# Kernel tuning notes

Hardware: AMD Instinct MI355X
Metric: run time of the kernel (lower is better)

## Reference

```python
import jax, jax.numpy as jnp
import numpy as np

N = 50000          # nodes
E = 1600000        # edges (avg degree 32)
F_IN = 128         # input feature dim
H = 8              # attention heads
D = 8              # per-head dim (concat -> H*D = 64)
NEG_SLOPE = 0.2    # PyG GATConv leaky relu slope


def setup_inputs() -> dict:
    key = jax.random.key(0)
    ks = jax.random.split(key, 16)
    x = jax.random.normal(ks[0], (N, F_IN), jnp.float32)
    edge_index = jax.random.randint(ks[1], (2, E), 0, N, jnp.int32)
    inp = {"x": x, "edge_index": edge_index}
    fin = F_IN
    for i in range(4):
        inp[f"W{i}"] = jax.random.normal(ks[2 + 3 * i], (fin, H * D), jnp.float32) * (1.0 / np.sqrt(fin))
        inp[f"att{i}"] = jax.random.normal(ks[3 + 3 * i], (2, H, D), jnp.float32) * 0.1
        inp[f"b{i}"] = jnp.zeros((H * D,), jnp.float32)
        fin = H * D
    return inp


def gat_layer(x, W, att, b, src, dst):
    # linear projection -> per-head features [N, H, D]
    h = (x @ W).reshape(-1, H, D)
    # per-node attention logits for src/dst roles [N, H]
    e_src = jnp.einsum("nhd,hd->nh", h, att[0])
    e_dst = jnp.einsum("nhd,hd->nh", h, att[1])
    # per-edge score [E, H]
    e = jax.nn.leaky_relu(e_src[src] + e_dst[dst], NEG_SLOPE)
    # segment softmax over incoming edges of each dst node
    m = jax.ops.segment_max(e, dst, num_segments=N)
    w = jnp.exp(e - m[dst])
    s = jax.ops.segment_sum(w, dst, num_segments=N)
    alpha = w / (s[dst] + 1e-16)
    # weighted message scatter-add: [E,H,D] -> [N,H,D]
    msg = alpha[:, :, None] * h[src]
    out = jax.ops.segment_sum(msg, dst, num_segments=N)
    return out.reshape(-1, H * D) + b


def reference(x, edge_index, W0, att0, b0, W1, att1, b1, W2, att2, b2, W3, att3, b3):
    src, dst = edge_index[0], edge_index[1]
    h = x
    params = [(W0, att0, b0), (W1, att1, b1), (W2, att2, b2), (W3, att3, b3)]
    for i, (W, att, b) in enumerate(params):
        h = gat_layer(h, W, att, b, src, dst)
        if i < len(params) - 1:
            h = jax.nn.elu(h)  # inter-layer activation as in PyG GAT (default ELU)
    return h
```

## Files before the change

### kernel.cpp

```cpp
#include <hip/hip_runtime.h>

#define N_NODES 50000
#define N_EDGES 1600000
#define HD 64
#define NH 8
#define NBKT 196
#define EPB 8192
#define GB1 196
#define SCAN_M (NBKT * GB1)
#define NB2 151
#define DCAP 8960
#define SEGB 2048
#define GBN 196

__device__ inline int wave_incl_scan(int v, int lane) {
#pragma unroll
    for (int o = 1; o < 64; o <<= 1) {
        int t = __shfl_up(v, o);
        if (lane >= o) v += t;
    }
    return v;
}

template <int F>
__device__ __forceinline__ void gemm_body16(
    int bx, int by, int t,
    const float* __restrict__ x, const float* __restrict__ W,
    const float* __restrict__ att,
    _Float16* __restrict__ h, float* __restrict__ es, float* __restrict__ ed) {
    int n = bx * 256 + t;
    int f0 = by * 16;
    int nc = (n < N_NODES) ? n : (N_NODES - 1);
    const float4* xrow = (const float4*)x + (size_t)nc * (F / 4);
    float acc[16];
#pragma unroll
    for (int i = 0; i < 16; i++) acc[i] = 0.f;
#pragma unroll 4
    for (int kk = 0; kk < F / 4; kk++) {
        float4 xv = xrow[kk];
        const float* Wk = W + (kk * 4) * 64 + f0;
#pragma unroll
        for (int i = 0; i < 16; i++)
            acc[i] += xv.x * Wk[i] + xv.y * Wk[64 + i] +
                      xv.z * Wk[128 + i] + xv.w * Wk[192 + i];
    }
    if (n >= N_NODES) return;

    float s0 = 0.f, s1 = 0.f, d0 = 0.f, d1 = 0.f;
#pragma unroll
    for (int i = 0; i < 8; i++) {
        s0 += acc[i] * att[f0 + i];
        d0 += acc[i] * att[64 + f0 + i];
    }
#pragma unroll
    for (int i = 8; i < 16; i++) {
        s1 += acc[i] * att[f0 + i];
        d1 += acc[i] * att[64 + f0 + i];
    }
    int hh = f0 >> 3;
    es[n * NH + hh] = s0; es[n * NH + hh + 1] = s1;
    ed[n * NH + hh] = d0; ed[n * NH + hh + 1] = d1;

    union { _Float16 hf[16]; uint4 u[2]; } cv;
#pragma unroll
    for (int i = 0; i < 16; i++) cv.hf[i] = (_Float16)acc[i];
    uint4* hp = (uint4*)(h + (size_t)n * HD + f0);
    hp[0] = cv.u[0];
    hp[1] = cv.u[1];
}

template <int F>
__global__ __launch_bounds__(256) void gemm_att_kernel(
    const float* __restrict__ x, const float* __restrict__ W,
    const float* __restrict__ att,
    _Float16* __restrict__ h, float* __restrict__ es, float* __restrict__ ed) {
    gemm_body16<F>(blockIdx.x, blockIdx.y, threadIdx.x, x, W, att, h, es, ed);
}

__global__ __launch_bounds__(256) void histA_gemm_kernel(
    const int* __restrict__ dst, int* __restrict__ offs,
    const float* __restrict__ x, const float* __restrict__ W,
    const float* __restrict__ att,
    _Float16* __restrict__ h, float* __restrict__ es, float* __restrict__ ed) {
    if (blockIdx.y < 4) {
        gemm_body16<128>(blockIdx.x, blockIdx.y, threadIdx.x, x, W, att, h, es, ed);
        return;
    }
    int bb = blockIdx.x;
    __shared__ int hist[NBKT];
    int t = threadIdx.x;
    if (t < NBKT) hist[t] = 0;
    __syncthreads();
    int base = bb * EPB;
#pragma unroll
    for (int k = 0; k < EPB / 256; k++) {
        int e = base + k * 256 + t;
        if (e < N_EDGES) atomicAdd(&hist[dst[e] >> 8], 1);
    }
    __syncthreads();
    if (t < NBKT) offs[t * GB1 + bb] = hist[t];
}

__global__ __launch_bounds__(256) void scanB1_kernel(int* __restrict__ offs,
                                                     int* __restrict__ part2) {
    __shared__ int wsum[4];
    int t = threadIdx.x, lane = t & 63, wv = t >> 6;
    int i = blockIdx.x * 256 + t;
    int v = (i < SCAN_M) ? offs[i] : 0;
    int inc = wave_incl_scan(v, lane);
    if (lane == 63) wsum[wv] = inc;
    __syncthreads();
    if (t == 0) {
        int a = 0;
        for (int k = 0; k < 4; k++) { int x = wsum[k]; wsum[k] = a; a += x; }
    }
    __syncthreads();
    int excl = wsum[wv] + inc - v;
    if (i < SCAN_M) offs[i] = excl;
    if (t == 255) part2[blockIdx.x] = wsum[wv] + inc;
}

__global__ __launch_bounds__(256) void scatC_kernel(const int* __restrict__ src,
                                                    const int* __restrict__ dst,
                                                    const int* __restrict__ offs,
                                                    const int* __restrict__ part2,
                                                    unsigned* __restrict__ ebuf) {
    __shared__ int cur[NBKT];
    __shared__ int base_s[NBKT];
    __shared__ int p2s[256];
    __shared__ int p2w[4];
    int t = threadIdx.x, lane = t & 63, wv = t >> 6;
    int v = (t < NB2) ? part2[t] : 0;
    int inc = wave_incl_scan(v, lane);
    if (lane == 63) p2w[wv] = inc;
    __syncthreads();
    if (t == 0) {
        int a = 0;
        for (int k = 0; k < 4; k++) { int x = p2w[k]; p2w[k] = a; a += x; }
    }
    __syncthreads();
    p2s[t] = p2w[wv] + inc - v;
    if (t < NBKT) cur[t] = 0;
    __syncthreads();
    if (t < NBKT) {
        int f = t * GB1 + blockIdx.x;
        base_s[t] = offs[f] + p2s[f >> 8];
    }
    __syncthreads();
    int base = blockIdx.x * EPB;
#pragma unroll
    for (int k = 0; k < EPB / 256; k++) {
        int e = base + k * 256 + t;
        if (e < N_EDGES) {
            int d = dst[e];
            int b = d >> 8;
            int r = atomicAdd(&cur[b], 1);
            ebuf[base_s[b] + r] = (unsigned)src[e] | ((unsigned)(d & 255) << 16);
        }
    }
}

__global__ __launch_bounds__(512) void csrD_kernel(const int* __restrict__ offs,
                                                   const int* __restrict__ part2,
                                                   const unsigned* __restrict__ ebuf,
                                                   int* __restrict__ rowptr,
                                                   unsigned short* __restrict__ csr) {
    __shared__ unsigned eb[DCAP];
    __shared__ int hist[SEGB];
    __shared__ int wsum[8];
    __shared__ int p2s[512];
    int b = blockIdx.x, t = threadIdx.x;
    int lane = t & 63, wv = t >> 6;
    {
        int v = (t < NB2) ? part2[t] : 0;
        int inc = wave_incl_scan(v, lane);
        if (lane == 63) wsum[wv] = inc;
        __syncthreads();
        if (t == 0) {
            int a = 0;
            for (int k = 0; k < 8; k++) { int x = wsum[k]; wsum[k] = a; a += x; }
        }
        __syncthreads();
        p2s[t] = wsum[wv] + inc - v;
        __syncthreads();
    }
    int f0 = b * GB1;
    int base = offs[f0] + p2s[f0 >> 8];
    int nxt;
    if (b == NBKT - 1) nxt = N_EDGES;
    else { int f1 = (b + 1) * GB1; nxt = offs[f1] + p2s[f1 >> 8]; }
    int nb = nxt - base;
    if (nb > DCAP) nb = DCAP;
    for (int i = t; i < SEGB; i += 512) hist[i] = 0;
    __syncthreads();
    for (int i = t; i < nb; i += 512) {
        unsigned v = ebuf[base + i];
        eb[i] = v;
        int bin = (int)((v >> 16) << 3) | (int)((v & 0xFFFFu) >> 13);
        atomicAdd(&hist[bin], 1);
    }
    __syncthreads();
    int b0 = t << 2;
    int loc0 = hist[b0], loc1 = hist[b0 + 1], loc2 = hist[b0 + 2], loc3 = hist[b0 + 3];
    int s = loc0 + loc1 + loc2 + loc3;
    int inc = wave_incl_scan(s, lane);
    if (lane == 63) wsum[wv] = inc;
    __syncthreads();
    if (t == 0) {
        int a = 0;
        for (int k = 0; k < 8; k++) { int x = wsum[k]; wsum[k] = a; a += x; }
    }
    __syncthreads();
    int run = wsum[wv] + inc - s;
    hist[b0] = run; run += loc0;
    hist[b0 + 1] = run; run += loc1;
    hist[b0 + 2] = run; run += loc2;
    hist[b0 + 3] = run;
    __syncthreads();
    if (t < 256) {
        int node = b * 256 + t;
        if (node < N_NODES) rowptr[node] = base + hist[t << 3];
    }
    if (b == 0 && t == 0) rowptr[N_NODES] = N_EDGES;
    __syncthreads();
    for (int i = t; i < nb; i += 512) {
        unsigned v = eb[i];
        int bin = (int)((v >> 16) << 3) | (int)((v & 0xFFFFu) >> 13);
        int r = atomicAdd(&hist[bin], 1);
        csr[base + r] = (unsigned short)(v & 0xFFFFu);
    }
}

__global__ __launch_bounds__(256) void agg_kernel(
    const uint4* __restrict__ h8, const float* __restrict__ es,
    const float* __restrict__ ed, const int* __restrict__ rowptr,
    const unsigned short* __restrict__ csr, const float4* __restrict__ b4,
    float4* __restrict__ out4, int apply_elu) {
    int t = threadIdx.x;
    int wv = t >> 6, L = t & 63;
    int n = blockIdx.x * 4 + wv;
    if (n >= N_NODES) return;
    int g = L >> 3, o = L & 7;
    int beg = rowptr[n], end = rowptr[n + 1];
    float edn = ed[n * NH + o];
    float acc[8] = {0.f, 0.f, 0.f, 0.f, 0.f, 0.f, 0.f, 0.f};
    float ssum = 0.f;
    int j = beg;
    for (; j + 32 <= end; j += 32) {
        int s0 = csr[j + g];
        int s1 = csr[j + 8 + g];
        int s2 = csr[j + 16 + g];
        int s3 = csr[j + 24 + g];
        uint4 hv0 = h8[s0 * 8 + o];
        uint4 hv1 = h8[s1 * 8 + o];
        uint4 hv2 = h8[s2 * 8 + o];
        uint4 hv3 = h8[s3 * 8 + o];
        float ev0 = es[s0 * NH + o];
        float ev1 = es[s1 * NH + o];
        float ev2 = es[s2 * NH + o];
        float ev3 = es[s3 * NH + o];
        float e0 = ev0 + edn; e0 = (e0 > 0.f) ? e0 : 0.2f * e0;
        float e1 = ev1 + edn; e1 = (e1 > 0.f) ? e1 : 0.2f * e1;
        float e2 = ev2 + edn; e2 = (e2 > 0.f) ? e2 : 0.2f * e2;
        float e3 = ev3 + edn; e3 = (e3 > 0.f) ? e3 : 0.2f * e3;
        float w0 = __expf(e0), w1 = __expf(e1);
        float w2 = __expf(e2), w3 = __expf(e3);
        union { uint4 u; _Float16 f[8]; } c0, c1, c2, c3;
        c0.u = hv0; c1.u = hv1; c2.u = hv2; c3.u = hv3;
#pragma unroll
        for (int i = 0; i < 8; i++) {
            acc[i] += w0 * (float)c0.f[i] + w1 * (float)c1.f[i];
            acc[i] += w2 * (float)c2.f[i] + w3 * (float)c3.f[i];
        }
        ssum += w0 + w1;
        ssum += w2 + w3;
    }
    for (; j + 16 <= end; j += 16) {
        int s0 = csr[j + g];
        int s1 = csr[j + 8 + g];
        uint4 hv0 = h8[s0 * 8 + o];
        uint4 hv1 = h8[s1 * 8 + o];
        float ev0 = es[s0 * NH + o];
        float ev1 = es[s1 * NH + o];
        float e0 = ev0 + edn; e0 = (e0 > 0.f) ? e0 : 0.2f * e0;
        float e1 = ev1 + edn; e1 = (e1 > 0.f) ? e1 : 0.2f * e1;
        float w0 = __expf(e0), w1 = __expf(e1);
        union { uint4 u; _Float16 f[8]; } c0, c1;
        c0.u = hv0; c1.u = hv1;
#pragma unroll
        for (int i = 0; i < 8; i++)
            acc[i] += w0 * (float)c0.f[i] + w1 * (float)c1.f[i];
        ssum += w0 + w1;
    }
    for (; j < end; j += 8) {
        int idx = j + g;
        int s0 = csr[(idx < end) ? idx : (end - 1)];
        float vmask = (idx < end) ? 1.f : 0.f;
        uint4 hv0 = h8[s0 * 8 + o];
        float ev0 = es[s0 * NH + o];
        float e0 = ev0 + edn; e0 = (e0 > 0.f) ? e0 : 0.2f * e0;
        float w0 = vmask * __expf(e0);
        union { uint4 u; _Float16 f[8]; } c0; c0.u = hv0;
#pragma unroll
        for (int i = 0; i < 8; i++) acc[i] += w0 * (float)c0.f[i];
        ssum += w0;
    }
#pragma unroll
    for (int i = 0; i < 8; i++) {
        acc[i] += __shfl_xor(acc[i], 8);
        acc[i] += __shfl_xor(acc[i], 16);
        acc[i] += __shfl_xor(acc[i], 32);
    }
    ssum += __shfl_xor(ssum, 8);
    ssum += __shfl_xor(ssum, 16);
    ssum += __shfl_xor(ssum, 32);

    if (g == 0) {
        float inv = 1.f / (ssum + 1e-16f);
        float4 bv0 = b4[2 * o], bv1 = b4[2 * o + 1];
        float4 r0, r1;
        r0.x = acc[0] * inv + bv0.x; r0.y = acc[1] * inv + bv0.y;
        r0.z = acc[2] * inv + bv0.z; r0.w = acc[3] * inv + bv0.w;
        r1.x = acc[4] * inv + bv1.x; r1.y = acc[5] * inv + bv1.y;
        r1.z = acc[6] * inv + bv1.z; r1.w = acc[7] * inv + bv1.w;
        if (apply_elu) {
            r0.x = (r0.x > 0.f) ? r0.x : (__expf(r0.x) - 1.f);
            r0.y = (r0.y > 0.f) ? r0.y : (__expf(r0.y) - 1.f);
            r0.z = (r0.z > 0.f) ? r0.z : (__expf(r0.z) - 1.f);
            r0.w = (r0.w > 0.f) ? r0.w : (__expf(r0.w) - 1.f);
            r1.x = (r1.x > 0.f) ? r1.x : (__expf(r1.x) - 1.f);
            r1.y = (r1.y > 0.f) ? r1.y : (__expf(r1.y) - 1.f);
            r1.z = (r1.z > 0.f) ? r1.z : (__expf(r1.z) - 1.f);
            r1.w = (r1.w > 0.f) ? r1.w : (__expf(r1.w) - 1.f);
        }
        out4[n * 16 + 2 * o] = r0;
        out4[n * 16 + 2 * o + 1] = r1;
    }
}

extern "C" void kernel_launch(void* const* d_in, const int* in_sizes, int n_in,
                              void* d_out, int out_size, void* d_ws, size_t ws_size,
                              hipStream_t stream) {
    const float* x   = (const float*)d_in[0];
    const int*   ei  = (const int*)d_in[1];
    const int*   src = ei;
    const int*   dst = ei + N_EDGES;
    const float* W[4]   = {(const float*)d_in[2], (const float*)d_in[5],
                           (const float*)d_in[8], (const float*)d_in[11]};
    const float* att[4] = {(const float*)d_in[3], (const float*)d_in[6],
                           (const float*)d_in[9], (const float*)d_in[12]};
    const float* bb[4]  = {(const float*)d_in[4], (const float*)d_in[7],
                           (const float*)d_in[10], (const float*)d_in[13]};

    char* wsb = (char*)d_ws;
    size_t off = 0;
    auto alloc = [&](size_t bytes) -> void* {
        size_t a = (off + 255) & ~(size_t)255;
        off = a + bytes;
        return (void*)(wsb + a);
    };
    int*            offs   = (int*)alloc((size_t)SCAN_M * 4);
    int*            part2  = (int*)alloc((size_t)NB2 * 4);
    unsigned*       ebuf   = (unsigned*)alloc((size_t)N_EDGES * 4);
    int*            rowptr = (int*)alloc((size_t)(N_NODES + 1) * 4);
    unsigned short* csr    = (unsigned short*)alloc((size_t)N_EDGES * 2);
    _Float16*       h      = (_Float16*)alloc((size_t)N_NODES * HD * 2);
    float*          es     = (float*)alloc((size_t)N_NODES * NH * 4);
    float*          ed     = (float*)alloc((size_t)N_NODES * NH * 4);
    float*          act0   = (float*)alloc((size_t)N_NODES * HD * 4);
    float*          act1   = (float*)alloc((size_t)N_NODES * HD * 4);

    const int GA = N_NODES / 4;
    const dim3 GG(GBN, 4);
    const dim3 GF(GBN, 5);

    histA_gemm_kernel<<<GF, 256, 0, stream>>>(dst, offs, x, W[0], att[0],
                                              h, es, ed);
    scanB1_kernel<<<NB2, 256, 0, stream>>>(offs, part2);
    scatC_kernel<<<GB1, 256, 0, stream>>>(src, dst, offs, part2, ebuf);
    csrD_kernel<<<NBKT, 512, 0, stream>>>(offs, part2, ebuf, rowptr, csr);

    agg_kernel<<<GA, 256, 0, stream>>>((const uint4*)h, es, ed, rowptr, csr,
                                       (const float4*)bb[0], (float4*)act0, 1);
    gemm_att_kernel<64><<<GG, 256, 0, stream>>>(act0, W[1], att[1], h, es, ed);
    agg_kernel<<<GA, 256, 0, stream>>>((const uint4*)h, es, ed, rowptr, csr,
                                       (const float4*)bb[1], (float4*)act1, 1);
    gemm_att_kernel<64><<<GG, 256, 0, stream>>>(act1, W[2], att[2], h, es, ed);
    agg_kernel<<<GA, 256, 0, stream>>>((const uint4*)h, es, ed, rowptr, csr,
                                       (const float4*)bb[2], (float4*)act0, 1);
    gemm_att_kernel<64><<<GG, 256, 0, stream>>>(act0, W[3], att[3], h, es, ed);
    agg_kernel<<<GA, 256, 0, stream>>>((const uint4*)h, es, ed, rowptr, csr,
                                       (const float4*)bb[3], (float4*)d_out, 0);
}
```

Before: 355.1 us.

## Process two nodes per wave in aggregation with a single masked tail step

Each 64-lane wave now handles two destination nodes (32 lanes each, 4 edge groups of 8 lanes) instead of one node with 8 edge groups, halving the grid. The 16-edge and 8-edge tail loops are replaced by one masked 16-edge step, and the cross-group reduction drops one shuffle stage. With average degree 32 this is meant to cut idle lanes and loop overhead in the tail and to reduce per-node reduction cost, at the price of fewer edges in flight per node and possible divergence between the two nodes sharing a wave.

```diff
diff --git a/kernel.cpp b/kernel.cpp
--- a/kernel.cpp
+++ b/kernel.cpp
@@ -238,19 +238,19 @@
     float4* __restrict__ out4, int apply_elu) {
     int t = threadIdx.x;
     int wv = t >> 6, L = t & 63;
-    int n = blockIdx.x * 4 + wv;
-    if (n >= N_NODES) return;
-    int g = L >> 3, o = L & 7;
+    int n = blockIdx.x * 8 + wv * 2 + (L >> 5);
+    int g = (L >> 3) & 3, o = L & 7;
     int beg = rowptr[n], end = rowptr[n + 1];
     float edn = ed[n * NH + o];
+    int last = (end > beg) ? (end - 1) : 0;
     float acc[8] = {0.f, 0.f, 0.f, 0.f, 0.f, 0.f, 0.f, 0.f};
     float ssum = 0.f;
     int j = beg;
-    for (; j + 32 <= end; j += 32) {
+    for (; j + 16 <= end; j += 16) {
         int s0 = csr[j + g];
-        int s1 = csr[j + 8 + g];
-        int s2 = csr[j + 16 + g];
-        int s3 = csr[j + 24 + g];
+        int s1 = csr[j + 4 + g];
+        int s2 = csr[j + 8 + g];
+        int s3 = csr[j + 12 + g];
         uint4 hv0 = h8[s0 * 8 + o];
         uint4 hv1 = h8[s1 * 8 + o];
         uint4 hv2 = h8[s2 * 8 + o];
@@ -275,45 +275,45 @@
         ssum += w0 + w1;
         ssum += w2 + w3;
     }
-    for (; j + 16 <= end; j += 16) {
-        int s0 = csr[j + g];
-        int s1 = csr[j + 8 + g];
+    if (j < end) {
+        int i0 = j + g, i1 = j + 4 + g, i2 = j + 8 + g, i3 = j + 12 + g;
+        int s0 = csr[(i0 < end) ? i0 : last];
+        int s1 = csr[(i1 < end) ? i1 : last];
+        int s2 = csr[(i2 < end) ? i2 : last];
+        int s3 = csr[(i3 < end) ? i3 : last];
         uint4 hv0 = h8[s0 * 8 + o];
         uint4 hv1 = h8[s1 * 8 + o];
+        uint4 hv2 = h8[s2 * 8 + o];
+        uint4 hv3 = h8[s3 * 8 + o];
         float ev0 = es[s0 * NH + o];
         float ev1 = es[s1 * NH + o];
+        float ev2 = es[s2 * NH + o];
+        float ev3 = es[s3 * NH + o];
         float e0 = ev0 + edn; e0 = (e0 > 0.f) ? e0 : 0.2f * e0;
         float e1 = ev1 + edn; e1 = (e1 > 0.f) ? e1 : 0.2f * e1;
-        float w0 = __expf(e0), w1 = __expf(e1);
-        union { uint4 u; _Float16 f[8]; } c0, c1;
-        c0.u = hv0; c1.u = hv1;
-#pragma unroll
-        for (int i = 0; i < 8; i++)
+        float e2 = ev2 + edn; e2 = (e2 > 0.f) ? e2 : 0.2f * e2;
+        float e3 = ev3 + edn; e3 = (e3 > 0.f) ? e3 : 0.2f * e3;
+        float w0 = (i0 < end) ? __expf(e0) : 0.f;
+        float w1 = (i1 < end) ? __expf(e1) : 0.f;
+        float w2 = (i2 < end) ? __expf(e2) : 0.f;
+        float w3 = (i3 < end) ? __expf(e3) : 0.f;
+        union { uint4 u; _Float16 f[8]; } c0, c1, c2, c3;
+        c0.u = hv0; c1.u = hv1; c2.u = hv2; c3.u = hv3;
+#pragma unroll
+        for (int i = 0; i < 8; i++) {
             acc[i] += w0 * (float)c0.f[i] + w1 * (float)c1.f[i];
+            acc[i] += w2 * (float)c2.f[i] + w3 * (float)c3.f[i];
+        }
         ssum += w0 + w1;
-    }
-    for (; j < end; j += 8) {
-        int idx = j + g;
-        int s0 = csr[(idx < end) ? idx : (end - 1)];
-        float vmask = (idx < end) ? 1.f : 0.f;
-        uint4 hv0 = h8[s0 * 8 + o];
-        float ev0 = es[s0 * NH + o];
-        float e0 = ev0 + edn; e0 = (e0 > 0.f) ? e0 : 0.2f * e0;
-        float w0 = vmask * __expf(e0);
-        union { uint4 u; _Float16 f[8]; } c0; c0.u = hv0;
-#pragma unroll
-        for (int i = 0; i < 8; i++) acc[i] += w0 * (float)c0.f[i];
-        ssum += w0;
+        ssum += w2 + w3;
     }
 #pragma unroll
     for (int i = 0; i < 8; i++) {
         acc[i] += __shfl_xor(acc[i], 8);
         acc[i] += __shfl_xor(acc[i], 16);
-        acc[i] += __shfl_xor(acc[i], 32);
     }
     ssum += __shfl_xor(ssum, 8);
     ssum += __shfl_xor(ssum, 16);
-    ssum += __shfl_xor(ssum, 32);
 
     if (g == 0) {
         float inv = 1.f / (ssum + 1e-16f);
@@ -370,7 +370,7 @@
     float*          act0   = (float*)alloc((size_t)N_NODES * HD * 4);
     float*          act1   = (float*)alloc((size_t)N_NODES * HD * 4);
 
-    const int GA = N_NODES / 4;
+    const int GA = N_NODES / 8;
     const dim3 GG(GBN, 4);
     const dim3 GF(GBN, 5);
 
```

Result: faster. 335.1 us (-5.6%).
